# Kernel optimization log

Measured on AMD Instinct MI355X. Metric: run time of the kernel, lower is better.

Reference implementation:

```python
import jax, jax.numpy as jnp
import numpy as np

N_NODES = 10000
N_EDGES = 160000
S1, V1 = 64, 32   # node irreps: 64x0e + 32x1e
S2, V2 = 16, 8    # edge irreps: 16x0e + 8x1e
N_GATE = V1       # one sigmoid gate scalar per output vector channel
S_OUT = S1 + N_GATE  # 96 scalar TP outputs (features + gates)
FAN_IN = 1280.0   # = S1*S2 + V1*V2 = S1*V2 + V1*S2 + V1*V2 (same for both outputs)
BN_EPS = 1e-5

# Levi-Civita tensor for the 1x1->1 (cross product) CG path
_lc = np.zeros((3, 3, 3), dtype=np.float32)
_lc[0, 1, 2] = _lc[1, 2, 0] = _lc[2, 0, 1] = 1.0
_lc[0, 2, 1] = _lc[2, 1, 0] = _lc[1, 0, 2] = -1.0
LC = jnp.asarray(_lc)


def setup_inputs() -> dict:
    key = jax.random.key(0)
    ks = jax.random.split(key, 8)
    return {
        'x': jax.random.normal(ks[0], (N_NODES, S1 + 3 * V1), dtype=jnp.float32),
        'edge_attr': jax.random.normal(ks[1], (N_EDGES, S2 + 3 * V2), dtype=jnp.float32),
        'W_ss': jax.random.normal(ks[2], (S1, S2, S_OUT), dtype=jnp.float32),
        'W_vv_s': jax.random.normal(ks[3], (V1, V2, S_OUT), dtype=jnp.float32),
        'W_sv': jax.random.normal(ks[4], (S1, V2, V1), dtype=jnp.float32),
        'W_vs': jax.random.normal(ks[5], (V1, S2, V1), dtype=jnp.float32),
        'W_vv_v': jax.random.normal(ks[6], (V1, V2, V1), dtype=jnp.float32),
        'bn_w_s': jnp.ones((S1,), dtype=jnp.float32),
        'bn_b_s': jnp.zeros((S1,), dtype=jnp.float32),
        'bn_w_v': jnp.ones((V1,), dtype=jnp.float32),
        'edge_index': jax.random.randint(ks[7], (2, N_EDGES), 0, N_NODES, dtype=jnp.int64),
    }


def reference(x, edge_attr, W_ss, W_vv_s, W_sv, W_vs, W_vv_v, bn_w_s, bn_b_s, bn_w_v, edge_index):
    i = edge_index[0]
    n = x.shape[0]

    # gather node features per edge; split into scalar / vector irreps
    xs = x[i]                                   # [E, 160]
    s1 = xs[:, :S1]                             # [E, 64]
    v1 = xs[:, S1:].reshape(-1, V1, 3)          # [E, 32, 3]
    s2 = edge_attr[:, :S2]                      # [E, 16]
    v2 = edge_attr[:, S2:].reshape(-1, V2, 3)   # [E, 8, 3]

    inv = 1.0 / np.sqrt(FAN_IN).astype(np.float32)

    # fully-connected equivariant tensor product (Clebsch-Gordan paths)
    s_out = (jnp.einsum('ea,eb,abc->ec', s1, s2, W_ss, optimize=True)
             + jnp.einsum('eam,ebm,abc->ec', v1, v2, W_vv_s, optimize=True) / np.sqrt(3.0)) * inv
    v_out = (jnp.einsum('ea,ebm,abc->ecm', s1, v2, W_sv, optimize=True)
             + jnp.einsum('eam,eb,abc->ecm', v1, s2, W_vs, optimize=True)
             + jnp.einsum('eam,ebn,mnp,abc->ecp', v1, v2, LC, W_vv_v, optimize=True) / np.sqrt(2.0)) * inv

    # swish gate: swish on feature scalars, sigmoid gates multiply vectors
    feat = jax.nn.silu(s_out[:, :S1])           # [E, 64]
    gate = jax.nn.sigmoid(s_out[:, S1:])        # [E, 32]
    v_g = v_out * gate[:, :, None]              # [E, 32, 3]

    # scatter-reduce (sum) back to nodes
    s_n = jax.ops.segment_sum(feat, i, num_segments=n)                             # [N, 64]
    v_n = jax.ops.segment_sum(v_g.reshape(-1, 3 * V1), i, num_segments=n).reshape(n, V1, 3)

    # equivariant batchnorm: standard BN on scalars, norm-only BN on vectors
    mu = s_n.mean(axis=0)
    var = jnp.mean((s_n - mu) ** 2, axis=0)
    s_bn = (s_n - mu) / jnp.sqrt(var + BN_EPS) * bn_w_s + bn_b_s
    vnorm = jnp.mean(jnp.sum(v_n ** 2, axis=-1), axis=0) / 3.0                     # [32]
    v_bn = v_n / jnp.sqrt(vnorm + BN_EPS)[None, :, None] * bn_w_v[None, :, None]

    # residual
    return jnp.concatenate([s_bn, v_bn.reshape(n, 3 * V1)], axis=-1) + x
```

## Files before the change

kernel.cpp:

```cpp
#include <hip/hip_runtime.h>
#include <hip/hip_bf16.h>


#define NNODES 10000
#define NEDGES 160000
#define EB 128
#define FSTRD 65

typedef unsigned short u16;
typedef unsigned int u32;
typedef short short8 __attribute__((ext_vector_type(8)));
typedef float f32x4 __attribute__((ext_vector_type(4)));

__device__ __forceinline__ u16 f2b(float f) {
  union { float f; u32 i; } v; v.f = f;
  u32 r = v.i + 0x7FFFu + ((v.i >> 16) & 1u);
  return (u16)(r >> 16);
}
__device__ __forceinline__ float lo_f(u32 d) {
  union { u32 i; float f; } v; v.i = d << 16; return v.f;
}
__device__ __forceinline__ float hi_f(u32 d) {
  union { u32 i; float f; } v; v.i = d & 0xFFFF0000u; return v.f;
}
__device__ __forceinline__ float qb(float f) {
  union { u32 i; float f; } v; v.i = ((u32)f2b(f)) << 16; return v.f;
}
__device__ __forceinline__ u32 pk2(float lo, float hi) {
  return __builtin_amdgcn_perm(__float_as_uint(hi), __float_as_uint(lo), 0x07060302u);
}
union frag_u { u32 w[4]; short8 s; };

#define INVF  0.02795084971874737f
#define INV3  0.5773502691896258f
#define INV2  0.7071067811865476f

__global__ void prep_kernel(const float* __restrict__ W_ss, const float* __restrict__ W_vv_s,
                            const float* __restrict__ W_sv, const float* __restrict__ W_vs,
                            const float* __restrict__ W_vv_v,
                            u32* __restrict__ WSd, u32* __restrict__ WVd,
                            float* __restrict__ zbase, int zcount) {
  int t = blockIdx.x * 256 + threadIdx.x;
  if (t < zcount) zbase[t] = 0.f;
  if (t < 61440) {
    int d = t;
    int nt = d / 10240, r = d - nt * 10240;
    int kt = r >> 8, l = (r & 255) >> 2, jp = r & 3;
    int n = nt * 16 + (l & 15);
    int k0 = kt * 32 + ((l >> 4) << 3) + jp * 2;
    float f0, f1;
    f0 = (k0     < 1024) ? W_ss[k0 * 96 + n] * INVF       : W_vv_s[(k0 - 1024) * 96 + n] * (INVF * INV3);
    f1 = (k0 + 1 < 1024) ? W_ss[(k0 + 1) * 96 + n] * INVF : W_vv_s[(k0 - 1023) * 96 + n] * (INVF * INV3);
    WSd[d] = (u32)f2b(f0) | ((u32)f2b(f1) << 16);
  } else if (t < 81920) {
    int d = t - 61440;
    int nt = d / 10240, r = d - nt * 10240;
    int kt = r >> 8, l = (r & 255) >> 2, jp = r & 3;
    int n = nt * 16 + (l & 15);
    int k0 = kt * 32 + ((l >> 4) << 3) + jp * 2;
    float f[2];
#pragma unroll
    for (int jj = 0; jj < 2; jj++) {
      int k = k0 + jj;
      if (k < 512)       f[jj] = W_sv[k * 32 + n] * INVF;
      else if (k < 1024) f[jj] = W_vs[(k - 512) * 32 + n] * INVF;
      else               f[jj] = W_vv_v[(k - 1024) * 32 + n] * (INVF * INV2);
    }
    WVd[d] = (u32)f2b(f[0]) | ((u32)f2b(f[1]) << 16);
  }
}

__global__ void count_kernel(const int* __restrict__ eidx, int* __restrict__ cnt) {
  int t = blockIdx.x * 256 + threadIdx.x;
  if (t < NEDGES) atomicAdd(&cnt[eidx[t]], 1);
}

__global__ void scan_kernel(const int* __restrict__ cnt, int* __restrict__ off,
                            int* __restrict__ cursor) {
  __shared__ int part[1024];
  int t = threadIdx.x;
  int local[10]; int s = 0;
  if (t < 1000) {
#pragma unroll
    for (int i = 0; i < 10; i++) { local[i] = cnt[t * 10 + i]; s += local[i]; }
  }
  part[t] = s; __syncthreads();
  for (int d = 1; d < 1024; d <<= 1) {
    int v = (t >= d) ? part[t - d] : 0; __syncthreads();
    part[t] += v; __syncthreads();
  }
  if (t < 1000) {
    int ex = (t == 0) ? 0 : part[t - 1];
#pragma unroll
    for (int i = 0; i < 10; i++) { off[t * 10 + i] = ex; cursor[t * 10 + i] = ex; ex += local[i]; }
  }
  if (t == 0) off[10000] = NEDGES;
}

__global__ void fill_kernel(const int* __restrict__ eidx, int* __restrict__ cursor,
                            int* __restrict__ elist) {
  int t = blockIdx.x * 256 + threadIdx.x;
  if (t < NEDGES) {
    int slot = atomicAdd(&cursor[eidx[t]], 1);
    elist[slot] = t;
  }
}

__global__ __launch_bounds__(256, 2) void edge_kernel(
    const float* __restrict__ x, const float* __restrict__ ea,
    const int* __restrict__ eidx,
    const u16* __restrict__ WSp, const u16* __restrict__ WVp,
    float* __restrict__ s_n, float* __restrict__ v_n,
    u16* __restrict__ msg16, int use_msg) {
  __shared__ int idxL[EB];
  __shared__ u32 fTd[160 * FSTRD];
  const int tid = threadIdx.x;
  const int eb = blockIdx.x * EB;

  if (tid < EB) idxL[tid] = eidx[eb + tid];
  __syncthreads();
#pragma unroll 1
  for (int t = tid; t < 64 * 160; t += 256) {
    int ep2 = t / 160, j = t - ep2 * 160;
    float vlo = x[(size_t)idxL[ep2] * 160 + j];
    float vhi = x[(size_t)idxL[ep2 + 64] * 160 + j];
    fTd[j * FSTRD + ep2] = (u32)f2b(vlo) | ((u32)f2b(vhi) << 16);
  }
  __syncthreads();

  const int wv = tid >> 6, lane = tid & 63;
  const int ln = lane & 15, quad = lane >> 4;
  const int ep = wv * 16 + ln;
  const int qh = quad >> 1, bb = (quad & 1) * 8;

  const float* eaL = ea + (size_t)(eb + ep) * 40;
  const float* eaH = eaL + 64 * 40;
  float s2l[8], s2h[8], v2l[24], v2h[24];
  {
    float4 a0 = *(const float4*)(eaL + bb), a1 = *(const float4*)(eaL + bb + 4);
    float4 b0 = *(const float4*)(eaH + bb), b1 = *(const float4*)(eaH + bb + 4);
    s2l[0]=qb(a0.x); s2l[1]=qb(a0.y); s2l[2]=qb(a0.z); s2l[3]=qb(a0.w);
    s2l[4]=qb(a1.x); s2l[5]=qb(a1.y); s2l[6]=qb(a1.z); s2l[7]=qb(a1.w);
    s2h[0]=qb(b0.x); s2h[1]=qb(b0.y); s2h[2]=qb(b0.z); s2h[3]=qb(b0.w);
    s2h[4]=qb(b1.x); s2h[5]=qb(b1.y); s2h[6]=qb(b1.z); s2h[7]=qb(b1.w);
#pragma unroll
    for (int i = 0; i < 6; i++) {
      float4 va = *(const float4*)(eaL + 16 + 4 * i);
      float4 vb = *(const float4*)(eaH + 16 + 4 * i);
      v2l[4*i+0]=qb(va.x); v2l[4*i+1]=qb(va.y); v2l[4*i+2]=qb(va.z); v2l[4*i+3]=qb(va.w);
      v2h[4*i+0]=qb(vb.x); v2h[4*i+1]=qb(vb.y); v2h[4*i+2]=qb(vb.z); v2h[4*i+3]=qb(vb.w);
    }
  }

  const u16* WS_l = WSp + (size_t)lane * 8;
  const u16* WV_l = WVp + (size_t)lane * 8;

#define LOAD_BS(B, ktv) { _Pragma("unroll") \
  for (int nt = 0; nt < 6; nt++) B[nt].s = *(const short8*)(WS_l + (size_t)(ktv) * 512 + nt * 20480); }
#define LOAD_BV(C, ktv) { _Pragma("unroll") \
  for (int nt = 0; nt < 2; nt++) C[nt].s = *(const short8*)(WV_l + (size_t)(ktv) * 512 + nt * 20480); }
#define MFMA_S(Al, Ah, B) { _Pragma("unroll") \
  for (int nt = 0; nt < 6; nt++) { \
    aS[0][nt] = __builtin_amdgcn_mfma_f32_16x16x32_bf16(Al.s, B[nt].s, aS[0][nt], 0, 0, 0); \
    aS[1][nt] = __builtin_amdgcn_mfma_f32_16x16x32_bf16(Ah.s, B[nt].s, aS[1][nt], 0, 0, 0); } }
#define MFMA_V(Al, Ah, C, p) { \
    aV[0][p][0] = __builtin_amdgcn_mfma_f32_16x16x32_bf16(Al.s, C[0].s, aV[0][p][0], 0, 0, 0); \
    aV[0][p][1] = __builtin_amdgcn_mfma_f32_16x16x32_bf16(Al.s, C[1].s, aV[0][p][1], 0, 0, 0); \
    aV[1][p][0] = __builtin_amdgcn_mfma_f32_16x16x32_bf16(Ah.s, C[0].s, aV[1][p][0], 0, 0, 0); \
    aV[1][p][1] = __builtin_amdgcn_mfma_f32_16x16x32_bf16(Ah.s, C[1].s, aV[1][p][1], 0, 0, 0); }

  f32x4 aS[2][6];
#pragma unroll
  for (int t = 0; t < 2; t++)
#pragma unroll
    for (int i = 0; i < 6; i++) aS[t][i] = (f32x4){0.f, 0.f, 0.f, 0.f};

  frag_u B0[6], B1[6];
  LOAD_BS(B0, 0);

#pragma unroll 1
  for (int c = 0; c < 16; c++) {
    int kt = 2 * c;
    u32 dA = fTd[(2 * kt + qh) * FSTRD + ep];
    u32 dB = fTd[(2 * kt + 2 + qh) * FSTRD + ep];
    LOAD_BS(B1, kt + 1);
    {
      frag_u Al, Ah;
      float slo = lo_f(dA), shi = hi_f(dA);
#pragma unroll
      for (int jp = 0; jp < 4; jp++) {
        Al.w[jp] = pk2(slo * s2l[2 * jp], slo * s2l[2 * jp + 1]);
        Ah.w[jp] = pk2(shi * s2h[2 * jp], shi * s2h[2 * jp + 1]);
      }
      MFMA_S(Al, Ah, B0);
    }
    LOAD_BS(B0, kt + 2);
    {
      frag_u Al, Ah;
      float slo = lo_f(dB), shi = hi_f(dB);
#pragma unroll
      for (int jp = 0; jp < 4; jp++) {
        Al.w[jp] = pk2(slo * s2l[2 * jp], slo * s2l[2 * jp + 1]);
        Ah.w[jp] = pk2(shi * s2h[2 * jp], shi * s2h[2 * jp + 1]);
      }
      MFMA_S(Al, Ah, B1);
    }
  }
#pragma unroll 1
  for (int c = 0; c < 4; c++) {
    int kt = 32 + 2 * c;
    int r0 = (64 + (4 * (kt - 32) + quad) * 3) * FSTRD + ep;
    int r1 = r0 + 12 * FSTRD;
    u32 d0 = fTd[r0], d1 = fTd[r0 + FSTRD], d2 = fTd[r0 + 2 * FSTRD];
    u32 e0 = fTd[r1], e1 = fTd[r1 + FSTRD], e2 = fTd[r1 + 2 * FSTRD];
    LOAD_BS(B1, kt + 1);
    {
      frag_u Al, Ah;
      float x0 = lo_f(d0), x1 = lo_f(d1), x2 = lo_f(d2);
      float y0 = hi_f(d0), y1 = hi_f(d1), y2 = hi_f(d2);
#pragma unroll
      for (int jp = 0; jp < 4; jp++) {
        int j0 = 6 * jp, j1 = 6 * jp + 3;
        Al.w[jp] = pk2(x0*v2l[j0] + x1*v2l[j0+1] + x2*v2l[j0+2],
                       x0*v2l[j1] + x1*v2l[j1+1] + x2*v2l[j1+2]);
        Ah.w[jp] = pk2(y0*v2h[j0] + y1*v2h[j0+1] + y2*v2h[j0+2],
                       y0*v2h[j1] + y1*v2h[j1+1] + y2*v2h[j1+2]);
      }
      MFMA_S(Al, Ah, B0);
    }
    LOAD_BS(B0, kt + 2);
    {
      frag_u Al, Ah;
      float x0 = lo_f(e0), x1 = lo_f(e1), x2 = lo_f(e2);
      float y0 = hi_f(e0), y1 = hi_f(e1), y2 = hi_f(e2);
#pragma unroll
      for (int jp = 0; jp < 4; jp++) {
        int j0 = 6 * jp, j1 = 6 * jp + 3;
        Al.w[jp] = pk2(x0*v2l[j0] + x1*v2l[j0+1] + x2*v2l[j0+2],
                       x0*v2l[j1] + x1*v2l[j1+1] + x2*v2l[j1+2]);
        Ah.w[jp] = pk2(y0*v2h[j0] + y1*v2h[j0+1] + y2*v2h[j0+2],
                       y0*v2h[j1] + y1*v2h[j1+1] + y2*v2h[j1+2]);
      }
      MFMA_S(Al, Ah, B1);
    }
  }

  frag_u C0[2], C1[2];
  LOAD_BV(C0, 32);

  float gateR[16];
#pragma unroll
  for (int t = 0; t < 2; t++) {
#pragma unroll
    for (int r = 0; r < 4; r++) {
      int er = wv * 16 + quad * 4 + r + t * 64;
      int nid = idxL[er];
#pragma unroll
      for (int nt = 0; nt < 6; nt++) {
        float v = aS[t][nt][r];
        float sg = 1.f / (1.f + __expf(-v));
        if (nt < 4) {
          if (use_msg) msg16[(size_t)(eb + er) * 160 + nt * 16 + ln] = f2b(v * sg);
          else         atomicAdd(&s_n[nid * 64 + nt * 16 + ln], v * sg);
        } else gateR[t * 8 + (nt - 4) * 4 + r] = sg;
      }
    }
  }

  f32x4 aV[2][3][2];
#pragma unroll
  for (int t = 0; t < 2; t++)
#pragma unroll
    for (int p = 0; p < 3; p++)
#pragma unroll
      for (int nt = 0; nt < 2; nt++) aV[t][p][nt] = (f32x4){0.f, 0.f, 0.f, 0.f};

#pragma unroll 1
  for (int c = 0; c < 4; c++) {
    int kt = 32 + 2 * c;
    int r0 = (64 + (4 * (kt - 32) + quad) * 3) * FSTRD + ep;
    int r1 = r0 + 12 * FSTRD;
    u32 d0 = fTd[r0], d1 = fTd[r0 + FSTRD], d2 = fTd[r0 + 2 * FSTRD];
    u32 e0 = fTd[r1], e1 = fTd[r1 + FSTRD], e2 = fTd[r1 + 2 * FSTRD];
    LOAD_BV(C1, kt + 1);
    {
      float wl[3] = { lo_f(d0), lo_f(d1), lo_f(d2) };
      float wh[3] = { hi_f(d0), hi_f(d1), hi_f(d2) };
#pragma unroll
      for (int p = 0; p < 3; p++) {
        const int p1 = (p + 1) % 3, p2 = (p + 2) % 3;
        frag_u Al, Ah;
#pragma unroll
        for (int jp = 0; jp < 4; jp++) {
          int j0 = 6 * jp, j1 = 6 * jp + 3;
          Al.w[jp] = pk2(wl[p1]*v2l[j0+p2] - wl[p2]*v2l[j0+p1],
                         wl[p1]*v2l[j1+p2] - wl[p2]*v2l[j1+p1]);
          Ah.w[jp] = pk2(wh[p1]*v2h[j0+p2] - wh[p2]*v2h[j0+p1],
                         wh[p1]*v2h[j1+p2] - wh[p2]*v2h[j1+p1]);
        }
        MFMA_V(Al, Ah, C0, p);
      }
    }
    LOAD_BV(C0, (c < 3) ? (kt + 2) : 0);
    {
      float wl[3] = { lo_f(e0), lo_f(e1), lo_f(e2) };
      float wh[3] = { hi_f(e0), hi_f(e1), hi_f(e2) };
#pragma unroll
      for (int p = 0; p < 3; p++) {
        const int p1 = (p + 1) % 3, p2 = (p + 2) % 3;
        frag_u Al, Ah;
#pragma unroll
        for (int jp = 0; jp < 4; jp++) {
          int j0 = 6 * jp, j1 = 6 * jp + 3;
          Al.w[jp] = pk2(wl[p1]*v2l[j0+p2] - wl[p2]*v2l[j0+p1],
                         wl[p1]*v2l[j1+p2] - wl[p2]*v2l[j1+p1]);
          Ah.w[jp] = pk2(wh[p1]*v2h[j0+p2] - wh[p2]*v2h[j0+p1],
                         wh[p1]*v2h[j1+p2] - wh[p2]*v2h[j1+p1]);
        }
        MFMA_V(Al, Ah, C1, p);
      }
    }
  }
#pragma unroll 1
  for (int c = 0; c < 8; c++) {
    int kt = 2 * c;
    u32 dA = fTd[(4 * kt + quad) * FSTRD + ep];
    u32 dB = fTd[(4 * kt + 4 + quad) * FSTRD + ep];
    LOAD_BV(C1, kt + 1);
    {
      float slo = lo_f(dA), shi = hi_f(dA);
#pragma unroll
      for (int p = 0; p < 3; p++) {
        frag_u Al, Ah;
#pragma unroll
        for (int jp = 0; jp < 4; jp++) {
          Al.w[jp] = pk2(slo * v2l[(2*jp)*3 + p], slo * v2l[(2*jp+1)*3 + p]);
          Ah.w[jp] = pk2(shi * v2h[(2*jp)*3 + p], shi * v2h[(2*jp+1)*3 + p]);
        }
        MFMA_V(Al, Ah, C0, p);
      }
    }
    LOAD_BV(C0, kt + 2);
    {
      float slo = lo_f(dB), shi = hi_f(dB);
#pragma unroll
      for (int p = 0; p < 3; p++) {
        frag_u Al, Ah;
#pragma unroll
        for (int jp = 0; jp < 4; jp++) {
          Al.w[jp] = pk2(slo * v2l[(2*jp)*3 + p], slo * v2l[(2*jp+1)*3 + p]);
          Ah.w[jp] = pk2(shi * v2h[(2*jp)*3 + p], shi * v2h[(2*jp+1)*3 + p]);
        }
        MFMA_V(Al, Ah, C1, p);
      }
    }
  }
#pragma unroll 1
  for (int c = 0; c < 8; c++) {
    int kt = 16 + 2 * c;
    int r0 = (64 + (2 * (kt - 16) + qh) * 3) * FSTRD + ep;
    int r1 = r0 + 6 * FSTRD;
    u32 d0 = fTd[r0], d1 = fTd[r0 + FSTRD], d2 = fTd[r0 + 2 * FSTRD];
    u32 e0 = fTd[r1], e1 = fTd[r1 + FSTRD], e2 = fTd[r1 + 2 * FSTRD];
    LOAD_BV(C1, kt + 1);
    {
      float vl[3] = { lo_f(d0), lo_f(d1), lo_f(d2) };
      float vh[3] = { hi_f(d0), hi_f(d1), hi_f(d2) };
#pragma unroll
      for (int p = 0; p < 3; p++) {
        frag_u Al, Ah;
#pragma unroll
        for (int jp = 0; jp < 4; jp++) {
          Al.w[jp] = pk2(vl[p] * s2l[2*jp], vl[p] * s2l[2*jp+1]);
          Ah.w[jp] = pk2(vh[p] * s2h[2*jp], vh[p] * s2h[2*jp+1]);
        }
        MFMA_V(Al, Ah, C0, p);
      }
    }
    LOAD_BV(C0, (c < 7) ? (kt + 2) : 0);
    {
      float vl[3] = { lo_f(e0), lo_f(e1), lo_f(e2) };
      float vh[3] = { hi_f(e0), hi_f(e1), hi_f(e2) };
#pragma unroll
      for (int p = 0; p < 3; p++) {
        frag_u Al, Ah;
#pragma unroll
        for (int jp = 0; jp < 4; jp++) {
          Al.w[jp] = pk2(vl[p] * s2l[2*jp], vl[p] * s2l[2*jp+1]);
          Ah.w[jp] = pk2(vh[p] * s2h[2*jp], vh[p] * s2h[2*jp+1]);
        }
        MFMA_V(Al, Ah, C1, p);
      }
    }
  }

#pragma unroll
  for (int t = 0; t < 2; t++) {
#pragma unroll
    for (int r = 0; r < 4; r++) {
      int er = wv * 16 + quad * 4 + r + t * 64;
      int nid = idxL[er];
#pragma unroll
      for (int nt = 0; nt < 2; nt++) {
        int c = nt * 16 + ln;
        float g = gateR[t * 8 + nt * 4 + r];
#pragma unroll
        for (int p = 0; p < 3; p++) {
          float val = aV[t][p][nt][r] * g;
          if (use_msg) msg16[(size_t)(eb + er) * 160 + 64 + c * 3 + p] = f2b(val);
          else         atomicAdd(&v_n[nid * 96 + c * 3 + p], val);
        }
      }
    }
  }
}

__global__ __launch_bounds__(256) void gather_kernel(
    const int* __restrict__ off, const int* __restrict__ elist,
    const u32* __restrict__ msg, float* __restrict__ s_n, float* __restrict__ v_n) {
  int tid = threadIdx.x;
  int n = blockIdx.x * 4 + (tid >> 6);
  int lane = tid & 63;
  int beg = off[n], end = off[n + 1];
  float a0 = 0.f, a1 = 0.f, b0 = 0.f, b1 = 0.f;
#pragma unroll 1
  for (int k0 = beg; k0 < end; k0 += 64) {
    int m = end - k0; if (m > 64) m = 64;
    int myE = (lane < m) ? elist[k0 + lane] : 0;
#pragma unroll 2
    for (int k = 0; k < m; k++) {
      int e = __shfl(myE, k);
      u32 w0 = msg[(size_t)e * 80 + lane];
      a0 += lo_f(w0); a1 += hi_f(w0);
      if (lane < 16) {
        u32 w1 = msg[(size_t)e * 80 + 64 + lane];
        b0 += lo_f(w1); b1 += hi_f(w1);
      }
    }
  }
  int ch = 2 * lane;
  if (ch < 64) {
    s_n[n * 64 + ch] = a0; s_n[n * 64 + ch + 1] = a1;
  } else {
    int q = ch - 64;
    v_n[n * 96 + q] = a0; v_n[n * 96 + q + 1] = a1;
  }
  if (lane < 16) {
    int q = 64 + 2 * lane;
    v_n[n * 96 + q] = b0; v_n[n * 96 + q + 1] = b1;
  }
}

__global__ void stats_kernel(const float* __restrict__ s_n, const float* __restrict__ v_n,
                             float* __restrict__ stats) {
  int b = blockIdx.x, tid = threadIdx.x;
  int r0 = b * 50;
  int c = tid & 63, rg = tid >> 6;
  float s = 0.f, sq = 0.f;
  for (int r = r0 + rg; r < r0 + 50; r += 4) {
    float v = s_n[r * 64 + c];
    s += v; sq += v * v;
  }
  atomicAdd(&stats[c], s);
  atomicAdd(&stats[64 + c], sq);
  int c2 = tid & 31, rg2 = tid >> 5;
  float vn = 0.f;
  for (int r = r0 + rg2; r < r0 + 50; r += 8) {
    const float* vp = &v_n[r * 96 + c2 * 3];
    vn += vp[0] * vp[0] + vp[1] * vp[1] + vp[2] * vp[2];
  }
  atomicAdd(&stats[128 + c2], vn);
}

__global__ void finalize_kernel(const float* __restrict__ s_n, const float* __restrict__ v_n,
                                const float* __restrict__ stats,
                                const float* __restrict__ x,
                                const float* __restrict__ bw_s, const float* __restrict__ bb_s,
                                const float* __restrict__ bw_v,
                                float* __restrict__ out) {
  int t = blockIdx.x * 256 + threadIdx.x;
  if (t >= NNODES * 160) return;
  int n = t / 160, j = t - n * 160;
  float xv = x[t];
  float r;
  if (j < 64) {
    float mu  = stats[j] * (1.f / NNODES);
    float var = stats[64 + j] * (1.f / NNODES) - mu * mu;
    var = fmaxf(var, 0.f);
    float v = s_n[n * 64 + j];
    r = (v - mu) * rsqrtf(var + 1e-5f) * bw_s[j] + bb_s[j];
  } else {
    int qq = j - 64;
    int c = qq / 3;
    float vn = stats[128 + c] * (1.f / (3.f * NNODES));
    float v = v_n[n * 96 + qq];
    r = v * rsqrtf(vn + 1e-5f) * bw_v[c];
  }
  out[t] = r + xv;
}

extern "C" void kernel_launch(void* const* d_in, const int* in_sizes, int n_in,
                              void* d_out, int out_size, void* d_ws, size_t ws_size,
                              hipStream_t stream) {
  const float* x      = (const float*)d_in[0];
  const float* ea     = (const float*)d_in[1];
  const float* W_ss   = (const float*)d_in[2];
  const float* W_vv_s = (const float*)d_in[3];
  const float* W_sv   = (const float*)d_in[4];
  const float* W_vs   = (const float*)d_in[5];
  const float* W_vv_v = (const float*)d_in[6];
  const float* bw_s   = (const float*)d_in[7];
  const float* bb_s   = (const float*)d_in[8];
  const float* bw_v   = (const float*)d_in[9];
  const int* eidx     = (const int*)d_in[10];
  float* out = (float*)d_out;

  float* ws    = (float*)d_ws;
  u16* WSp     = (u16*)d_ws;
  u16* WVp     = WSp + 122880;
  float* s_n   = ws + 81920;
  float* v_n   = s_n + 640000;
  float* stats = v_n + 960000;
  int* cnt     = (int*)(ws + 1682080);
  int* off     = (int*)(ws + 1692080);
  int* cursor  = (int*)(ws + 1702084);
  int* elist   = (int*)(ws + 1712084);
  u32* msg     = (u32*)(ws + 1872084);

  int use_msg = (ws_size >= 58688336ULL) ? 1 : 0;

  if (use_msg) {
    prep_kernel<<<6251, 256, 0, stream>>>(W_ss, W_vv_s, W_sv, W_vs, W_vv_v,
                                          (u32*)WSp, (u32*)WVp, stats, 10160);
    count_kernel<<<625, 256, 0, stream>>>(eidx, cnt);
    scan_kernel<<<1, 1024, 0, stream>>>(cnt, off, cursor);
    fill_kernel<<<625, 256, 0, stream>>>(eidx, cursor, elist);
  } else {
    prep_kernel<<<6251, 256, 0, stream>>>(W_ss, W_vv_s, W_sv, W_vs, W_vv_v,
                                          (u32*)WSp, (u32*)WVp, s_n, 1600160);
  }
  edge_kernel<<<NEDGES / EB, 256, 0, stream>>>(x, ea, eidx, WSp, WVp, s_n, v_n,
                                               (u16*)msg, use_msg);
  if (use_msg)
    gather_kernel<<<2500, 256, 0, stream>>>(off, elist, msg, s_n, v_n);
  stats_kernel<<<200, 256, 0, stream>>>(s_n, v_n, stats);
  finalize_kernel<<<(NNODES * 160 + 255) / 256, 256, 0, stream>>>(
      s_n, v_n, stats, x, bw_s, bb_s, bw_v, out);
}
```

Before: 374.1 us.

## Process edges in destination-sorted order so gather reads messages contiguously

The edge kernel now takes edges in the CSR order built by count/scan/fill. Each block therefore works on edges grouped by destination node. Messages are written in that sorted order, so the gather kernel streams one contiguous range per node instead of doing indirect lookups through the edge list, and node-feature gathers of x hit repeated rows. In exchange, edge_attr rows are now read through an indirection. The count pass is folded into the prep kernel and the zeroing moves to hipMemsetAsync, removing one launch.

```diff
diff --git a/kernel.cpp b/kernel.cpp
--- a/kernel.cpp
+++ b/kernel.cpp
@@ -39,9 +39,10 @@
                             const float* __restrict__ W_sv, const float* __restrict__ W_vs,
                             const float* __restrict__ W_vv_v,
                             u32* __restrict__ WSd, u32* __restrict__ WVd,
-                            float* __restrict__ zbase, int zcount) {
+                            const int* __restrict__ eidx, int* __restrict__ cnt,
+                            int do_count) {
   int t = blockIdx.x * 256 + threadIdx.x;
-  if (t < zcount) zbase[t] = 0.f;
+  if (do_count && t < NEDGES) atomicAdd(&cnt[eidx[t]], 1);
   if (t < 61440) {
     int d = t;
     int nt = d / 10240, r = d - nt * 10240;
@@ -70,11 +71,6 @@
   }
 }
 
-__global__ void count_kernel(const int* __restrict__ eidx, int* __restrict__ cnt) {
-  int t = blockIdx.x * 256 + threadIdx.x;
-  if (t < NEDGES) atomicAdd(&cnt[eidx[t]], 1);
-}
-
 __global__ void scan_kernel(const int* __restrict__ cnt, int* __restrict__ off,
                             int* __restrict__ cursor) {
   __shared__ int part[1024];
@@ -108,16 +104,21 @@
 
 __global__ __launch_bounds__(256, 2) void edge_kernel(
     const float* __restrict__ x, const float* __restrict__ ea,
-    const int* __restrict__ eidx,
+    const int* __restrict__ eidx, const int* __restrict__ elist,
     const u16* __restrict__ WSp, const u16* __restrict__ WVp,
     float* __restrict__ s_n, float* __restrict__ v_n,
     u16* __restrict__ msg16, int use_msg) {
   __shared__ int idxL[EB];
+  __shared__ int eoL[EB];
   __shared__ u32 fTd[160 * FSTRD];
   const int tid = threadIdx.x;
   const int eb = blockIdx.x * EB;
 
-  if (tid < EB) idxL[tid] = eidx[eb + tid];
+  if (tid < EB) {
+    int eo = use_msg ? elist[eb + tid] : (eb + tid);
+    eoL[tid] = eo;
+    idxL[tid] = eidx[eo];
+  }
   __syncthreads();
 #pragma unroll 1
   for (int t = tid; t < 64 * 160; t += 256) {
@@ -133,8 +134,8 @@
   const int ep = wv * 16 + ln;
   const int qh = quad >> 1, bb = (quad & 1) * 8;
 
-  const float* eaL = ea + (size_t)(eb + ep) * 40;
-  const float* eaH = eaL + 64 * 40;
+  const float* eaL = ea + (size_t)eoL[ep] * 40;
+  const float* eaH = ea + (size_t)eoL[ep + 64] * 40;
   float s2l[8], s2h[8], v2l[24], v2h[24];
   {
     float4 a0 = *(const float4*)(eaL + bb), a1 = *(const float4*)(eaL + bb + 4);
@@ -416,26 +417,20 @@
 }
 
 __global__ __launch_bounds__(256) void gather_kernel(
-    const int* __restrict__ off, const int* __restrict__ elist,
-    const u32* __restrict__ msg, float* __restrict__ s_n, float* __restrict__ v_n) {
+    const int* __restrict__ off, const u32* __restrict__ msg,
+    float* __restrict__ s_n, float* __restrict__ v_n) {
   int tid = threadIdx.x;
   int n = blockIdx.x * 4 + (tid >> 6);
   int lane = tid & 63;
   int beg = off[n], end = off[n + 1];
   float a0 = 0.f, a1 = 0.f, b0 = 0.f, b1 = 0.f;
-#pragma unroll 1
-  for (int k0 = beg; k0 < end; k0 += 64) {
-    int m = end - k0; if (m > 64) m = 64;
-    int myE = (lane < m) ? elist[k0 + lane] : 0;
 #pragma unroll 2
-    for (int k = 0; k < m; k++) {
-      int e = __shfl(myE, k);
-      u32 w0 = msg[(size_t)e * 80 + lane];
-      a0 += lo_f(w0); a1 += hi_f(w0);
-      if (lane < 16) {
-        u32 w1 = msg[(size_t)e * 80 + 64 + lane];
-        b0 += lo_f(w1); b1 += hi_f(w1);
-      }
+  for (int k = beg; k < end; k++) {
+    u32 w0 = msg[(size_t)k * 80 + lane];
+    a0 += lo_f(w0); a1 += hi_f(w0);
+    if (lane < 16) {
+      u32 w1 = msg[(size_t)k * 80 + 64 + lane];
+      b0 += lo_f(w1); b1 += hi_f(w1);
     }
   }
   int ch = 2 * lane;
@@ -530,19 +525,21 @@
   int use_msg = (ws_size >= 58688336ULL) ? 1 : 0;
 
   if (use_msg) {
-    prep_kernel<<<6251, 256, 0, stream>>>(W_ss, W_vv_s, W_sv, W_vs, W_vv_v,
-                                          (u32*)WSp, (u32*)WVp, stats, 10160);
-    count_kernel<<<625, 256, 0, stream>>>(eidx, cnt);
+    hipMemsetAsync(stats, 0, 160 * sizeof(float), stream);
+    hipMemsetAsync(cnt, 0, NNODES * sizeof(int), stream);
+    prep_kernel<<<625, 256, 0, stream>>>(W_ss, W_vv_s, W_sv, W_vs, W_vv_v,
+                                         (u32*)WSp, (u32*)WVp, eidx, cnt, 1);
     scan_kernel<<<1, 1024, 0, stream>>>(cnt, off, cursor);
     fill_kernel<<<625, 256, 0, stream>>>(eidx, cursor, elist);
   } else {
-    prep_kernel<<<6251, 256, 0, stream>>>(W_ss, W_vv_s, W_sv, W_vs, W_vv_v,
-                                          (u32*)WSp, (u32*)WVp, s_n, 1600160);
-  }
-  edge_kernel<<<NEDGES / EB, 256, 0, stream>>>(x, ea, eidx, WSp, WVp, s_n, v_n,
-                                               (u16*)msg, use_msg);
+    hipMemsetAsync(s_n, 0, 1600160 * sizeof(float), stream);
+    prep_kernel<<<625, 256, 0, stream>>>(W_ss, W_vv_s, W_sv, W_vs, W_vv_v,
+                                         (u32*)WSp, (u32*)WVp, eidx, cnt, 0);
+  }
+  edge_kernel<<<NEDGES / EB, 256, 0, stream>>>(x, ea, eidx, elist, WSp, WVp,
+                                               s_n, v_n, (u16*)msg, use_msg);
   if (use_msg)
-    gather_kernel<<<2500, 256, 0, stream>>>(off, elist, msg, s_n, v_n);
+    gather_kernel<<<2500, 256, 0, stream>>>(off, msg, s_n, v_n);
   stats_kernel<<<200, 256, 0, stream>>>(s_n, v_n, stats);
   finalize_kernel<<<(NNODES * 160 + 255) / 256, 256, 0, stream>>>(
       s_n, v_n, stats, x, bw_s, bb_s, bw_v, out);
```

Measured after the change: 373.2 us. No clear change (-0.2%).
